# Kernel optimization log

Hardware: AMD Instinct MI355X
Metric: run time of the kernel (lower is better)

Reference implementation:

```python
import jax, jax.numpy as jnp
import numpy as np

N, DIN, D, H, L, S, E = 3072, 64, 128, 4, 2, 4, 49152
NEG = -2.0**32 + 1.0


def _layernorm(x, g, b, eps=1e-5):
    m = jnp.mean(x, axis=-1, keepdims=True)
    v = jnp.var(x, axis=-1, keepdims=True)
    return (x - m) * jax.lax.rsqrt(v + eps) * g + b


def setup_inputs() -> dict:
    key = jax.random.key(0)
    ks = jax.random.split(key, 24)
    w = lambda k, shp: (0.02 * jax.random.normal(k, shp)).astype(jnp.float32)
    inp = {
        "x": jax.random.normal(ks[0], (N, DIN), dtype=jnp.float32),
        "edge_index": jax.random.randint(ks[1], (2, E), 0, N, dtype=jnp.int64) if jax.config.jax_enable_x64 else jax.random.randint(ks[1], (2, E), 0, N).astype(jnp.int32),
        "shortest_path_len": jax.random.randint(ks[2], (N, N), 0, 11).astype(jnp.int32),
        "edge_feat": jax.random.normal(ks[3], (N, N, S), dtype=jnp.float32),
        # input projection
        "node_W": w(ks[4], (DIN, D)), "node_b": jnp.zeros((D,), jnp.float32),
        # centrality / spatial / edge encodings
        "deg_emb": w(ks[5], (N, D)),
        "sp_emb": w(ks[6], (11, 1)),
        "edge_W": w(ks[7], (S, S)), "edge_b": jnp.zeros((S,), jnp.float32),
        # per-layer stacked attention params
        "ln1_g": jnp.ones((L, D), jnp.float32), "ln1_b": jnp.zeros((L, D), jnp.float32),
        "Wq": w(ks[8], (L, H, D, D)), "bq": jnp.zeros((L, H, D), jnp.float32),
        "Wk": w(ks[9], (L, H, D, D)), "bk": jnp.zeros((L, H, D), jnp.float32),
        "Wv": w(ks[10], (L, H, D, D)), "bv": jnp.zeros((L, H, D), jnp.float32),
        "Wo": w(ks[11], (L, H * D, D)), "bo": jnp.zeros((L, D), jnp.float32),
        "ln2_g": jnp.ones((L, D), jnp.float32), "ln2_b": jnp.zeros((L, D), jnp.float32),
        "ff_W": w(ks[12], (L, D, D)), "ff_b": jnp.zeros((L, D), jnp.float32),
        # output projection
        "out_W": w(ks[13], (D, D)), "out_b": jnp.zeros((D,), jnp.float32),
    }
    return inp


def reference(x, edge_index, shortest_path_len, edge_feat,
              node_W, node_b, deg_emb, sp_emb, edge_W, edge_b,
              ln1_g, ln1_b, Wq, bq, Wk, bk, Wv, bv, Wo, bo,
              ln2_g, ln2_b, ff_W, ff_b, out_W, out_b):
    # padding mask from raw features
    mask_idx = (jnp.sum(x, axis=1) != 0).astype(x.dtype)            # [N]
    mask = mask_idx[:, None] * mask_idx[None, :]                    # [N,N]

    h = x @ node_W + node_b                                         # [N,D]
    # centrality: degree of edge destinations
    deg = jax.ops.segment_sum(jnp.ones((edge_index.shape[1],), jnp.int32),
                              edge_index[1], num_segments=N)        # [N]
    h = h + deg_emb[deg]

    spatial = sp_emb[shortest_path_len][..., 0]                     # [N,N]
    edge_m = (edge_feat @ edge_W + edge_b).mean(axis=-1)            # [N,N]
    bias = spatial + edge_m
    scale = 1.0 / jnp.sqrt(jnp.asarray(D, x.dtype))

    for l in range(L):
        x_ln = _layernorm(h, ln1_g[l], ln1_b[l])                    # [N,D]
        q = jnp.einsum('nd,hdk->hnk', x_ln, Wq[l]) + bq[l][:, None, :]
        k = jnp.einsum('nd,hdk->hnk', x_ln, Wk[l]) + bk[l][:, None, :]
        v = jnp.einsum('nd,hdk->hnk', x_ln, Wv[l]) + bv[l][:, None, :]
        a = jnp.einsum('hnk,hmk->hnm', q, k) * scale + bias[None]   # [H,N,N]
        a = jnp.where(mask[None] == 0, NEG, a)
        s = jax.nn.softmax(a, axis=-1)
        s = jnp.where(mask[None] == 0, 0.0, s)
        o = jnp.einsum('hnm,hmd->hnd', s, v)                        # [H,N,D]
        cat = jnp.transpose(o, (1, 0, 2)).reshape(N, H * D)         # [N,H*D]
        x_out = cat @ Wo[l] + bo[l] + h
        h = _layernorm(x_out, ln2_g[l], ln2_b[l]) @ ff_W[l] + ff_b[l] + x_out

    return h @ out_W + out_b
```

## Files before the change

kernel.cpp:

```cpp
#include <hip/hip_runtime.h>
#include <math.h>

static constexpr int N   = 3072;
static constexpr int DIN = 64;
static constexpr int D   = 128;
static constexpr int H   = 4;
static constexpr int E   = 49152;
#define NEGV  (-4294967295.0f)
#define SCALE (0.08838834764831845f)

typedef unsigned short u16;
typedef __attribute__((ext_vector_type(8))) short short8;
typedef __attribute__((ext_vector_type(4))) float f32x4;
typedef __attribute__((ext_vector_type(4))) unsigned short u16x4;

__device__ __forceinline__ u16 f2bf(float f){
  unsigned int u = __float_as_uint(f);
  u += 0x7fff + ((u >> 16) & 1);
  return (u16)(u >> 16);
}
__device__ __forceinline__ float bf2f(u16 u){
  return __uint_as_float(((unsigned int)u) << 16);
}

__global__ void k_zero_deg(int* __restrict__ deg){
  int i = blockIdx.x*blockDim.x + threadIdx.x;
  if(i < N) deg[i] = 0;
}

__global__ void k_deg(const int* __restrict__ ei, int* __restrict__ deg){
  int e = blockIdx.x*blockDim.x + threadIdx.x;
  if(e < E) atomicAdd(&deg[ei[E + e]], 1);
}

__global__ void k_h0(const float* __restrict__ x, const float* __restrict__ nodeW,
                     const float* __restrict__ nodeb, const float* __restrict__ degemb,
                     const int* __restrict__ deg, const float* __restrict__ g1,
                     const float* __restrict__ b1, float* __restrict__ mask,
                     float* __restrict__ h, float* __restrict__ xln){
  const int i = blockIdx.x, t = threadIdx.x;
  float xv = x[i*DIN + t];
  float s = xv;
  #pragma unroll
  for(int o=32;o;o>>=1) s += __shfl_xor(s, o);
  if(t == 0) mask[i] = (s != 0.0f) ? 1.0f : 0.0f;
  __shared__ float xr[DIN];
  xr[t] = xv;
  __syncthreads();
  int dg = deg[i]; dg = dg > N-1 ? N-1 : dg;
  float a0 = nodeb[t]      + degemb[dg*D + t];
  float a1 = nodeb[t + 64] + degemb[dg*D + t + 64];
  #pragma unroll
  for(int u=0; u<DIN; ++u){
    float xu = xr[u];
    a0 = fmaf(xu, nodeW[u*D + t],      a0);
    a1 = fmaf(xu, nodeW[u*D + t + 64], a1);
  }
  h[i*D + t]      = a0;
  h[i*D + t + 64] = a1;
  float s2 = a0 + a1, sq = a0*a0 + a1*a1;
  #pragma unroll
  for(int o=32;o;o>>=1){ s2 += __shfl_xor(s2, o); sq += __shfl_xor(sq, o); }
  float mean = s2*(1.0f/128.0f);
  float var  = sq*(1.0f/128.0f) - mean*mean;
  float inv  = rsqrtf(var + 1e-5f);
  xln[i*D + t]      = (a0 - mean)*inv*g1[t]      + b1[t];
  xln[i*D + t + 64] = (a1 - mean)*inv*g1[t + 64] + b1[t + 64];
}

__global__ void k_bias(const int* __restrict__ spl, const float* __restrict__ ef,
                       const float* __restrict__ spe, const float* __restrict__ eW,
                       const float* __restrict__ eb, const float* __restrict__ mask,
                       u16* __restrict__ biasm){
  int idx = blockIdx.x*blockDim.x + threadIdx.x;
  int i = idx / N, j = idx % N;
  float wm0 = (eW[0] + eW[1] + eW[2] + eW[3])  * 0.25f;
  float wm1 = (eW[4] + eW[5] + eW[6] + eW[7])  * 0.25f;
  float wm2 = (eW[8] + eW[9] + eW[10]+ eW[11]) * 0.25f;
  float wm3 = (eW[12]+ eW[13]+ eW[14]+ eW[15]) * 0.25f;
  float bm  = (eb[0] + eb[1] + eb[2] + eb[3])  * 0.25f;
  float4 e4 = reinterpret_cast<const float4*>(ef)[idx];
  float em = fmaf(e4.x, wm0, fmaf(e4.y, wm1, fmaf(e4.z, wm2, fmaf(e4.w, wm3, bm))));
  float b = spe[spl[idx]] + em;
  float mk = mask[i]*mask[j];
  biasm[idx] = f2bf((mk != 0.0f) ? b : NEGV);
}

__global__ __launch_bounds__(256) void k_wt_all(const float* __restrict__ Wq, const float* __restrict__ Wk,
    const float* __restrict__ Wv, const float* __restrict__ ffW, const float* __restrict__ outW,
    u16* __restrict__ wt_qkv, u16* __restrict__ wt_ff, u16* __restrict__ wt_out){
  __shared__ float t[32][33];
  const int z = blockIdx.y;
  const float* src; u16* dst;
  if(z < 24){
    int l = z/12, r = z%12;
    const float* W = (r>>2)==0 ? Wq : (r>>2)==1 ? Wk : Wv;
    src = W + (size_t)(l*4 + (r&3))*16384;
    dst = wt_qkv + (size_t)z*16384;
  } else if(z < 26){
    src = ffW + (size_t)(z-24)*16384; dst = wt_ff + (size_t)(z-24)*16384;
  } else { src = outW; dst = wt_out; }
  const int ki = blockIdx.x & 3, ni = blockIdx.x >> 2;
  const int tid = threadIdx.x;
  #pragma unroll
  for(int i=0;i<4;i++){
    int idx = tid + i*256, r = idx>>5, c = idx&31;
    t[r][c] = src[(size_t)(ki*32+r)*128 + ni*32 + c];
  }
  __syncthreads();
  #pragma unroll
  for(int i=0;i<4;i++){
    int idx = tid + i*256, r = idx>>5, c = idx&31;
    dst[(size_t)(ni*32+r)*128 + ki*32 + c] = f2bf(t[c][r]);
  }
}

__global__ __launch_bounds__(256) void k_wt_wo(const float* __restrict__ Wo, u16* __restrict__ wt_wo){
  __shared__ float t[32][33];
  const int l = blockIdx.y;
  const float* src = Wo + (size_t)l*65536;
  u16* dst = wt_wo + (size_t)l*65536;
  const int ki = blockIdx.x & 15, ni = blockIdx.x >> 4;
  const int tid = threadIdx.x;
  #pragma unroll
  for(int i=0;i<4;i++){
    int idx = tid + i*256, r = idx>>5, c = idx&31;
    t[r][c] = src[(size_t)(ki*32+r)*128 + ni*32 + c];
  }
  __syncthreads();
  #pragma unroll
  for(int i=0;i<4;i++){
    int idx = tid + i*256, r = idx>>5, c = idx&31;
    dst[(size_t)(ni*32+r)*512 + ki*32 + c] = f2bf(t[c][r]);
  }
}

template<int MODE>
__device__ __forceinline__ void mgemm_body(const float* __restrict__ A, const u16* __restrict__ Bt,
                                           const float* __restrict__ bias, void* __restrict__ Cv){
  __shared__ u16 As[64*128];
  __shared__ u16 Bs[128*128];
  const int tid = threadIdx.x, w = tid>>6, lane = tid&63;
  const int g4 = lane>>4, l16 = lane&15;
  const int m0 = blockIdx.x*64;
  const int srow = tid>>4, sch = tid&15;
  f32x4 acc[8];
  #pragma unroll
  for(int nt=0;nt<8;++nt) acc[nt] = (f32x4){0.f,0.f,0.f,0.f};
  #pragma unroll
  for(int it=0;it<4;++it){
    int row = it*16 + srow;
    const float4* ap = reinterpret_cast<const float4*>(A + (size_t)(m0+row)*128 + sch*8);
    float4 x0 = ap[0], x1 = ap[1];
    u16x4 p0, p1;
    p0.x=f2bf(x0.x); p0.y=f2bf(x0.y); p0.z=f2bf(x0.z); p0.w=f2bf(x0.w);
    p1.x=f2bf(x1.x); p1.y=f2bf(x1.y); p1.z=f2bf(x1.z); p1.w=f2bf(x1.w);
    u16* dst = &As[row*128 + ((sch ^ (row&15))*8)];
    *reinterpret_cast<u16x4*>(dst)     = p0;
    *reinterpret_cast<u16x4*>(dst + 4) = p1;
  }
  #pragma unroll
  for(int it=0;it<8;++it){
    int row = it*16 + srow;
    short8 b = *reinterpret_cast<const short8*>(Bt + (size_t)row*128 + sch*8);
    *reinterpret_cast<short8*>(&Bs[row*128 + ((sch ^ (row&15))*8)]) = b;
  }
  __syncthreads();
  __builtin_amdgcn_s_setprio(1);
  #pragma unroll
  for(int c=0;c<4;++c){
    short8 af = *reinterpret_cast<const short8*>(&As[(w*16+l16)*128 + (((c*4+g4) ^ l16)*8)]);
    #pragma unroll
    for(int nt=0;nt<8;++nt){
      short8 bf = *reinterpret_cast<const short8*>(&Bs[(nt*16+l16)*128 + (((c*4+g4) ^ l16)*8)]);
      acc[nt] = __builtin_amdgcn_mfma_f32_16x16x32_bf16(af, bf, acc[nt], 0, 0, 0);
    }
  }
  __builtin_amdgcn_s_setprio(0);
  const int mrow = m0 + w*16 + g4*4;
  if(MODE == 2){
    __syncthreads();
    u16* T = Bs;
    #pragma unroll
    for(int nt=0;nt<8;++nt){
      const int col = nt*16 + l16;
      float bi = bias[col];
      u16x4 t;
      t.x = f2bf(acc[nt][0] + bi); t.y = f2bf(acc[nt][1] + bi);
      t.z = f2bf(acc[nt][2] + bi); t.w = f2bf(acc[nt][3] + bi);
      *reinterpret_cast<u16x4*>(&T[col*68 + (w*16 + g4*4)]) = t;
    }
    __syncthreads();
    #pragma unroll
    for(int i=0;i<4;++i){
      int slot = tid + i*256;
      int col = slot >> 3, q = slot & 7;
      short8 v = *reinterpret_cast<const short8*>(&T[col*68 + q*8]);
      *reinterpret_cast<short8*>((u16*)Cv + (size_t)col*N + m0 + q*8) = v;
    }
  } else {
    #pragma unroll
    for(int nt=0;nt<8;++nt){
      const int col = nt*16 + l16;
      float bi = bias[col];
      #pragma unroll
      for(int rg=0;rg<4;++rg){
        float v = acc[nt][rg] + bi;
        ((u16*)Cv)[(size_t)(mrow+rg)*128 + col] = f2bf(v);
      }
    }
  }
}

__global__ __launch_bounds__(256) void k_mqkv(const float* __restrict__ xln, const u16* __restrict__ wt_qkv,
    const float* __restrict__ bq, const float* __restrict__ bk, const float* __restrict__ bv,
    u16* __restrict__ q, u16* __restrict__ k, u16* __restrict__ vT, int l){
  const int z = blockIdx.y, which = z>>2, head = z&3;
  const u16* Bt = wt_qkv + (size_t)(l*12 + z)*16384;
  if(which == 0)      mgemm_body<1>(xln, Bt, bq + (l*H+head)*D, q  + (size_t)head*N*D);
  else if(which == 1) mgemm_body<1>(xln, Bt, bk + (l*H+head)*D, k  + (size_t)head*N*D);
  else                mgemm_body<2>(xln, Bt, bv + (l*H+head)*D, vT + (size_t)head*N*D);
}

template<int S, bool LAST>
__global__ __launch_bounds__(256) void k_mwoff(const u16* __restrict__ opart, const float* __restrict__ mpart,
    const float* __restrict__ lpart, const float* __restrict__ mask, const u16* __restrict__ wt_wo_l,
    const float* __restrict__ bo_l, const float* __restrict__ hres,
    const u16* __restrict__ wt_ff_l, const float* __restrict__ ffb_l,
    const float* __restrict__ g2, const float* __restrict__ b2,
    float* __restrict__ hout, float* __restrict__ xlnout,
    const float* __restrict__ g1n, const float* __restrict__ b1n,
    const u16* __restrict__ wt_out_m, const float* __restrict__ outb_m,
    float* __restrict__ finalout){
  __shared__ u16 As[64*128];
  __shared__ u16 Bs[128*128];
  const int tid = threadIdx.x, w = tid>>6, lane = tid&63;
  const int g4 = lane>>4, l16 = lane&15;
  const int m0 = blockIdx.x*64;
  const int srow = tid>>4, sch = tid&15;
  f32x4 acc[8];
  #pragma unroll
  for(int nt=0;nt<8;++nt) acc[nt] = (f32x4){0.f,0.f,0.f,0.f};
  for(int k0 = 0; k0 < 512; k0 += 128){
    const int hh = k0 >> 7;
    __syncthreads();
    #pragma unroll
    for(int it=0;it<4;++it){
      int row = it*16 + srow;
      int grow = m0 + row;
      float w_[S]; float M = -INFINITY; float mv[S], lv[S];
      #pragma unroll
      for(int s=0;s<S;++s){
        mv[s] = mpart[(size_t)(s*H + hh)*N + grow];
        lv[s] = lpart[(size_t)(s*H + hh)*N + grow];
        M = fmaxf(M, mv[s]);
      }
      float denom = 0.f;
      #pragma unroll
      for(int s=0;s<S;++s){ w_[s] = __expf(mv[s] - M); denom = fmaf(lv[s], w_[s], denom); }
      float scale = mask[grow] / denom;
      const int d = sch*8;
      float v[8] = {0,0,0,0,0,0,0,0};
      #pragma unroll
      for(int s=0;s<S;++s){
        short8 ov = *reinterpret_cast<const short8*>(
            opart + ((size_t)(s*H + hh)*N + grow)*D + d);
        #pragma unroll
        for(int j=0;j<8;++j) v[j] = fmaf(bf2f((u16)ov[j]), w_[s], v[j]);
      }
      u16x4 p0, p1;
      p0.x=f2bf(v[0]*scale); p0.y=f2bf(v[1]*scale); p0.z=f2bf(v[2]*scale); p0.w=f2bf(v[3]*scale);
      p1.x=f2bf(v[4]*scale); p1.y=f2bf(v[5]*scale); p1.z=f2bf(v[6]*scale); p1.w=f2bf(v[7]*scale);
      u16* dst = &As[row*128 + ((sch ^ (row&15))*8)];
      *reinterpret_cast<u16x4*>(dst)     = p0;
      *reinterpret_cast<u16x4*>(dst + 4) = p1;
    }
    #pragma unroll
    for(int it=0;it<8;++it){
      int row = it*16 + srow;
      short8 b = *reinterpret_cast<const short8*>(wt_wo_l + (size_t)row*512 + k0 + sch*8);
      *reinterpret_cast<short8*>(&Bs[row*128 + ((sch ^ (row&15))*8)]) = b;
    }
    __syncthreads();
    __builtin_amdgcn_s_setprio(1);
    #pragma unroll
    for(int c=0;c<4;++c){
      short8 af = *reinterpret_cast<const short8*>(&As[(w*16+l16)*128 + (((c*4+g4) ^ l16)*8)]);
      #pragma unroll
      for(int nt=0;nt<8;++nt){
        short8 bf = *reinterpret_cast<const short8*>(&Bs[(nt*16+l16)*128 + (((c*4+g4) ^ l16)*8)]);
        acc[nt] = __builtin_amdgcn_mfma_f32_16x16x32_bf16(af, bf, acc[nt], 0, 0, 0);
      }
    }
    __builtin_amdgcn_s_setprio(0);
  }
  const int mrow = m0 + w*16 + g4*4;
  float s_[4] = {0,0,0,0}, q_[4] = {0,0,0,0};
  #pragma unroll
  for(int nt=0;nt<8;++nt){
    const int col = nt*16 + l16;
    float bi = bo_l[col];
    #pragma unroll
    for(int rg=0;rg<4;++rg){
      float v = acc[nt][rg] + bi + hres[(size_t)(mrow+rg)*128 + col];
      acc[nt][rg] = v;
      s_[rg] += v; q_[rg] = fmaf(v, v, q_[rg]);
    }
  }
  #pragma unroll
  for(int o=1;o<16;o<<=1){
    #pragma unroll
    for(int rg=0;rg<4;++rg){ s_[rg] += __shfl_xor(s_[rg], o); q_[rg] += __shfl_xor(q_[rg], o); }
  }
  float mean[4], inv[4];
  #pragma unroll
  for(int rg=0;rg<4;++rg){
    mean[rg] = s_[rg]*(1.0f/128.0f);
    float var = q_[rg]*(1.0f/128.0f) - mean[rg]*mean[rg];
    inv[rg] = rsqrtf(var + 1e-5f);
  }
  __syncthreads();
  #pragma unroll
  for(int nt=0;nt<8;++nt){
    const int col = nt*16 + l16;
    const int ch = col >> 3, wi = col & 7;
    float gg = g2[col], bb = b2[col];
    #pragma unroll
    for(int rg=0;rg<4;++rg){
      int row = w*16 + g4*4 + rg;
      As[row*128 + ((ch ^ (row&15))*8) + wi] = f2bf((acc[nt][rg] - mean[rg])*inv[rg]*gg + bb);
    }
  }
  #pragma unroll
  for(int it=0;it<8;++it){
    int row = it*16 + srow;
    short8 b = *reinterpret_cast<const short8*>(wt_ff_l + (size_t)row*128 + sch*8);
    *reinterpret_cast<short8*>(&Bs[row*128 + ((sch ^ (row&15))*8)]) = b;
  }
  __syncthreads();
  f32x4 acc2[8];
  #pragma unroll
  for(int nt=0;nt<8;++nt) acc2[nt] = (f32x4){0.f,0.f,0.f,0.f};
  __builtin_amdgcn_s_setprio(1);
  #pragma unroll
  for(int c=0;c<4;++c){
    short8 af = *reinterpret_cast<const short8*>(&As[(w*16+l16)*128 + (((c*4+g4) ^ l16)*8)]);
    #pragma unroll
    for(int nt=0;nt<8;++nt){
      short8 bf = *reinterpret_cast<const short8*>(&Bs[(nt*16+l16)*128 + (((c*4+g4) ^ l16)*8)]);
      acc2[nt] = __builtin_amdgcn_mfma_f32_16x16x32_bf16(af, bf, acc2[nt], 0, 0, 0);
    }
  }
  __builtin_amdgcn_s_setprio(0);
  #pragma unroll
  for(int nt=0;nt<8;++nt){
    const int col = nt*16 + l16;
    float bi = ffb_l[col];
    #pragma unroll
    for(int rg=0;rg<4;++rg)
      acc2[nt][rg] += bi + acc[nt][rg];
  }
  if(!LAST){
    float s2_[4] = {0,0,0,0}, q2_[4] = {0,0,0,0};
    #pragma unroll
    for(int nt=0;nt<8;++nt){
      const int col = nt*16 + l16;
      #pragma unroll
      for(int rg=0;rg<4;++rg){
        float v = acc2[nt][rg];
        hout[(size_t)(mrow+rg)*128 + col] = v;
        s2_[rg] += v; q2_[rg] = fmaf(v, v, q2_[rg]);
      }
    }
    #pragma unroll
    for(int o=1;o<16;o<<=1){
      #pragma unroll
      for(int rg=0;rg<4;++rg){ s2_[rg] += __shfl_xor(s2_[rg], o); q2_[rg] += __shfl_xor(q2_[rg], o); }
    }
    #pragma unroll
    for(int rg=0;rg<4;++rg){
      float mn = s2_[rg]*(1.0f/128.0f);
      float var = q2_[rg]*(1.0f/128.0f) - mn*mn;
      s2_[rg] = mn; q2_[rg] = rsqrtf(var + 1e-5f);
    }
    #pragma unroll
    for(int nt=0;nt<8;++nt){
      const int col = nt*16 + l16;
      float gg = g1n[col], bb = b1n[col];
      #pragma unroll
      for(int rg=0;rg<4;++rg)
        xlnout[(size_t)(mrow+rg)*128 + col] = (acc2[nt][rg] - s2_[rg])*q2_[rg]*gg + bb;
    }
  } else {
    __syncthreads();
    #pragma unroll
    for(int nt=0;nt<8;++nt){
      const int col = nt*16 + l16;
      const int ch = col >> 3, wi = col & 7;
      #pragma unroll
      for(int rg=0;rg<4;++rg){
        int row = w*16 + g4*4 + rg;
        As[row*128 + ((ch ^ (row&15))*8) + wi] = f2bf(acc2[nt][rg]);
      }
    }
    #pragma unroll
    for(int it=0;it<8;++it){
      int row = it*16 + srow;
      short8 b = *reinterpret_cast<const short8*>(wt_out_m + (size_t)row*128 + sch*8);
      *reinterpret_cast<short8*>(&Bs[row*128 + ((sch ^ (row&15))*8)]) = b;
    }
    __syncthreads();
    f32x4 acc3[8];
    #pragma unroll
    for(int nt=0;nt<8;++nt) acc3[nt] = (f32x4){0.f,0.f,0.f,0.f};
    __builtin_amdgcn_s_setprio(1);
    #pragma unroll
    for(int c=0;c<4;++c){
      short8 af = *reinterpret_cast<const short8*>(&As[(w*16+l16)*128 + (((c*4+g4) ^ l16)*8)]);
      #pragma unroll
      for(int nt=0;nt<8;++nt){
        short8 bf = *reinterpret_cast<const short8*>(&Bs[(nt*16+l16)*128 + (((c*4+g4) ^ l16)*8)]);
        acc3[nt] = __builtin_amdgcn_mfma_f32_16x16x32_bf16(af, bf, acc3[nt], 0, 0, 0);
      }
    }
    __builtin_amdgcn_s_setprio(0);
    #pragma unroll
    for(int nt=0;nt<8;++nt){
      const int col = nt*16 + l16;
      float bi = outb_m[col];
      #pragma unroll
      for(int rg=0;rg<4;++rg)
        finalout[(size_t)(mrow+rg)*128 + col] = acc3[nt][rg] + bi;
    }
  }
}

__global__ __launch_bounds__(256) void k_attn(const u16* __restrict__ q, const u16* __restrict__ k,
                     const u16* __restrict__ vT, const u16* __restrict__ biasm,
                     u16* __restrict__ opart, float* __restrict__ mpart, float* __restrict__ lpart,
                     int kvlen){
  const int tid  = threadIdx.x;
  const int w    = tid >> 6;
  const int lane = tid & 63;
  const int g4 = lane >> 4, l16 = lane & 15;
  const int head = blockIdx.y, sp = blockIdx.z;
  const int r0 = blockIdx.x*64 + w*16;
  __shared__ u16 Ks[64*128];
  __shared__ u16 Vs[64*128];
  __shared__ u16 P[4][16][40];

  const u16* qbase = q + ((size_t)head*N + r0)*D;
  short8 qf[4];
  #pragma unroll
  for(int c=0;c<4;c++)
    qf[c] = *reinterpret_cast<const short8*>(qbase + l16*D + c*32 + g4*8);

  f32x4 o[8];
  #pragma unroll
  for(int dt=0;dt<8;dt++) o[dt] = (f32x4){0.f,0.f,0.f,0.f};
  float m = -INFINITY, lsum = 0.0f;

  const u16* kh   = k  + (size_t)head*N*D;
  const u16* vTh  = vT + (size_t)head*D*N;
  const u16* brow = biasm + (size_t)(r0 + l16)*N;
  const int kv0 = sp*kvlen;

  const int krow = tid >> 4, kch = tid & 15;
  const int vrow = tid >> 3, vch = tid & 7;

  for(int j0 = kv0; j0 < kv0 + kvlen; j0 += 64){
    short8 kreg[4], vreg[4];
    #pragma unroll
    for(int it=0; it<4; ++it)
      kreg[it] = *reinterpret_cast<const short8*>(kh + (size_t)(j0 + it*16 + krow)*D + kch*8);
    #pragma unroll
    for(int it=0; it<4; ++it)
      vreg[it] = *reinterpret_cast<const short8*>(vTh + (size_t)(it*32 + vrow)*N + j0 + vch*8);
    u16x4 bb[4];
    #pragma unroll
    for(int z=0; z<4; ++z)
      bb[z] = *reinterpret_cast<const u16x4*>(brow + j0 + z*16 + g4*4);

    __syncthreads();
    #pragma unroll
    for(int it=0; it<4; ++it){
      int row = it*16 + krow;
      *reinterpret_cast<short8*>(&Ks[row*128 + ((kch ^ (row&15))*8)]) = kreg[it];
    }
    #pragma unroll
    for(int it=0; it<4; ++it){
      int d = it*32 + vrow;
      int row = d & 63, ch = ((d>>6)<<3) | vch;
      *reinterpret_cast<short8*>(&Vs[row*128 + ((ch ^ (row&15))*8)]) = vreg[it];
    }
    __syncthreads();

    #pragma unroll
    for(int ks=0; ks<2; ++ks){
      short8 kf[8];
      const int rowA = ks*32 + l16, rowB = rowA + 16;
      #pragma unroll
      for(int c=0;c<4;c++){
        kf[c]   = *reinterpret_cast<const short8*>(&Ks[rowA*128 + (((c*4+g4) ^ l16)*8)]);
        kf[4+c] = *reinterpret_cast<const short8*>(&Ks[rowB*128 + (((c*4+g4) ^ l16)*8)]);
      }
      f32x4 sA = (f32x4){0.f,0.f,0.f,0.f}, sB = sA;
      __builtin_amdgcn_s_setprio(1);
      #pragma unroll
      for(int c=0;c<4;c++){
        sA = __builtin_amdgcn_mfma_f32_16x16x32_bf16(kf[c],   qf[c], sA, 0, 0, 0);
        sB = __builtin_amdgcn_mfma_f32_16x16x32_bf16(kf[4+c], qf[c], sB, 0, 0, 0);
      }
      __builtin_amdgcn_s_setprio(0);
      u16x4 bA = bb[2*ks], bB = bb[2*ks+1];
      sA[0] = fmaf(sA[0], SCALE, bf2f(bA.x)); sA[1] = fmaf(sA[1], SCALE, bf2f(bA.y));
      sA[2] = fmaf(sA[2], SCALE, bf2f(bA.z)); sA[3] = fmaf(sA[3], SCALE, bf2f(bA.w));
      sB[0] = fmaf(sB[0], SCALE, bf2f(bB.x)); sB[1] = fmaf(sB[1], SCALE, bf2f(bB.y));
      sB[2] = fmaf(sB[2], SCALE, bf2f(bB.z)); sB[3] = fmaf(sB[3], SCALE, bf2f(bB.w));
      float pmax = fmaxf(fmaxf(fmaxf(sA[0],sA[1]), fmaxf(sA[2],sA[3])),
                         fmaxf(fmaxf(sB[0],sB[1]), fmaxf(sB[2],sB[3])));
      pmax = fmaxf(pmax, __shfl_xor(pmax, 16));
      pmax = fmaxf(pmax, __shfl_xor(pmax, 32));
      if(!__all(pmax - m <= 8.0f)){
        float mnew = fmaxf(m, pmax);
        float corr = __expf(m - mnew);
        lsum *= corr;
        float c0 = __shfl(corr, (lane & 48) | (g4*4 + 0));
        float c1 = __shfl(corr, (lane & 48) | (g4*4 + 1));
        float c2 = __shfl(corr, (lane & 48) | (g4*4 + 2));
        float c3 = __shfl(corr, (lane & 48) | (g4*4 + 3));
        #pragma unroll
        for(int dt=0;dt<8;dt++){
          o[dt][0] *= c0; o[dt][1] *= c1; o[dt][2] *= c2; o[dt][3] *= c3;
        }
        m = mnew;
      }
      f32x4 pA, pB;
      #pragma unroll
      for(int rg=0;rg<4;rg++){ pA[rg] = __expf(sA[rg] - m); pB[rg] = __expf(sB[rg] - m); }
      float ps = (pA[0]+pA[1]) + (pA[2]+pA[3]) + ((pB[0]+pB[1]) + (pB[2]+pB[3]));
      ps += __shfl_xor(ps, 16);
      ps += __shfl_xor(ps, 32);
      lsum += ps;
      u16x4 wa, wb;
      wa.x = f2bf(pA[0]); wa.y = f2bf(pA[1]); wa.z = f2bf(pA[2]); wa.w = f2bf(pA[3]);
      wb.x = f2bf(pB[0]); wb.y = f2bf(pB[1]); wb.z = f2bf(pB[2]); wb.w = f2bf(pB[3]);
      *reinterpret_cast<u16x4*>(&P[w][l16][g4*4])      = wa;
      *reinterpret_cast<u16x4*>(&P[w][l16][16 + g4*4]) = wb;
      short8 pf = *reinterpret_cast<const short8*>(&P[w][l16][g4*8]);
      __builtin_amdgcn_s_setprio(1);
      #pragma unroll
      for(int dt=0;dt<8;dt++){
        int d = dt*16 + l16;
        int row = d & 63;
        int ch  = ((dt>>2)<<3) | (ks<<2) | g4;
        short8 vf = *reinterpret_cast<const short8*>(&Vs[row*128 + ((ch ^ l16)*8)]);
        o[dt] = __builtin_amdgcn_mfma_f32_16x16x32_bf16(pf, vf, o[dt], 0, 0, 0);
      }
      __builtin_amdgcn_s_setprio(0);
    }
  }

  u16* ob = opart + ((size_t)((sp*H + head)*N) + r0)*D;
  #pragma unroll
  for(int dt=0;dt<8;dt++){
    #pragma unroll
    for(int rg=0;rg<4;rg++)
      ob[(size_t)(g4*4+rg)*D + dt*16 + l16] = f2bf(o[dt][rg]);
  }
  if(g4 == 0){
    mpart[(size_t)(sp*H + head)*N + r0 + l16] = m;
    lpart[(size_t)(sp*H + head)*N + r0 + l16] = lsum;
  }
}

extern "C" void kernel_launch(void* const* d_in, const int* in_sizes, int n_in,
                              void* d_out, int out_size, void* d_ws, size_t ws_size,
                              hipStream_t stream){
  const float* x      = (const float*)d_in[0];
  const int*   ei     = (const int*)  d_in[1];
  const int*   spl    = (const int*)  d_in[2];
  const float* ef     = (const float*)d_in[3];
  const float* nodeW  = (const float*)d_in[4];
  const float* nodeb  = (const float*)d_in[5];
  const float* degemb = (const float*)d_in[6];
  const float* spe    = (const float*)d_in[7];
  const float* eW     = (const float*)d_in[8];
  const float* eb     = (const float*)d_in[9];
  const float* ln1g   = (const float*)d_in[10];
  const float* ln1b   = (const float*)d_in[11];
  const float* Wq     = (const float*)d_in[12];
  const float* bq     = (const float*)d_in[13];
  const float* Wk     = (const float*)d_in[14];
  const float* bk     = (const float*)d_in[15];
  const float* Wv     = (const float*)d_in[16];
  const float* bv     = (const float*)d_in[17];
  const float* Wo     = (const float*)d_in[18];
  const float* bo     = (const float*)d_in[19];
  const float* ln2g   = (const float*)d_in[20];
  const float* ln2b   = (const float*)d_in[21];
  const float* ffW    = (const float*)d_in[22];
  const float* ffb    = (const float*)d_in[23];
  const float* outW   = (const float*)d_in[24];
  const float* outb   = (const float*)d_in[25];

  constexpr size_t WT_ELEMS = 24*16384 + 2*16384 + 16384 + 2*65536;
  auto needed = [](int s)->size_t{
    size_t fl = 8192 + 3*(size_t)N*D;
    size_t bf = 3*(size_t)H*N*D + (size_t)N*N + (size_t)s*H*N*D;
    size_t pf = 2*(size_t)s*H*N;
    return fl*4 + bf*2 + pf*4 + WT_ELEMS*2;
  };
  int S = 2;
  if(needed(8) <= ws_size) S = 8;
  else if(needed(4) <= ws_size) S = 4;

  float* ws   = (float*)d_ws;
  int*   deg  = (int*)ws;
  float* mask = ws + 4096;
  float* h    = ws + 8192;
  float* xln  = h    + N*D;
  float* xout = xln  + N*D;
  u16*   qb   = (u16*)(xout + N*D);
  u16*   kb   = qb + (size_t)H*N*D;
  u16*   vTb  = kb + (size_t)H*N*D;
  u16*   biasm= vTb + (size_t)H*N*D;
  u16*   opart= biasm + (size_t)N*N;
  float* mpart= (float*)(opart + (size_t)S*H*N*D);
  float* lpart= mpart + (size_t)S*H*N;
  u16*   wt_qkv = (u16*)(lpart + (size_t)S*H*N);
  u16*   wt_ff  = wt_qkv + 24*16384;
  u16*   wt_out = wt_ff  + 2*16384;
  u16*   wt_wo  = wt_out + 16384;

  k_wt_all<<<dim3(16, 27), 256, 0, stream>>>(Wq, Wk, Wv, ffW, outW, wt_qkv, wt_ff, wt_out);
  k_wt_wo<<<dim3(64, 2), 256, 0, stream>>>(Wo, wt_wo);
  k_zero_deg<<<(N+255)/256, 256, 0, stream>>>(deg);
  k_deg<<<(E+255)/256, 256, 0, stream>>>(ei, deg);
  k_h0<<<N, 64, 0, stream>>>(x, nodeW, nodeb, degemb, deg, ln1g, ln1b, mask, h, xln);
  k_bias<<<(N*N)/256, 256, 0, stream>>>(spl, ef, spe, eW, eb, mask, biasm);

  for(int l = 0; l < 2; ++l){
    k_mqkv<<<dim3(N/64, 12), 256, 0, stream>>>(xln, wt_qkv, bq, bk, bv, qb, kb, vTb, l);
    k_attn<<<dim3(N/64, H, S), 256, 0, stream>>>(qb, kb, vTb, biasm, opart, mpart, lpart, N/S);
    const u16* wwo = wt_wo + (size_t)l*65536;
    const u16* wff = wt_ff + (size_t)l*16384;
    if(l == 0){
      if(S == 8)
        k_mwoff<8,false><<<N/64, 256, 0, stream>>>(opart, mpart, lpart, mask, wwo, bo + l*D, h,
            wff, ffb + l*D, ln2g + l*D, ln2b + l*D, h, xln, ln1g + D, ln1b + D,
            nullptr, nullptr, nullptr);
      else if(S == 4)
        k_mwoff<4,false><<<N/64, 256, 0, stream>>>(opart, mpart, lpart, mask, wwo, bo + l*D, h,
            wff, ffb + l*D, ln2g + l*D, ln2b + l*D, h, xln, ln1g + D, ln1b + D,
            nullptr, nullptr, nullptr);
      else
        k_mwoff<2,false><<<N/64, 256, 0, stream>>>(opart, mpart, lpart, mask, wwo, bo + l*D, h,
            wff, ffb + l*D, ln2g + l*D, ln2b + l*D, h, xln, ln1g + D, ln1b + D,
            nullptr, nullptr, nullptr);
    } else {
      if(S == 8)
        k_mwoff<8,true><<<N/64, 256, 0, stream>>>(opart, mpart, lpart, mask, wwo, bo + l*D, h,
            wff, ffb + l*D, ln2g + l*D, ln2b + l*D, nullptr, nullptr, nullptr, nullptr,
            wt_out, outb, (float*)d_out);
      else if(S == 4)
        k_mwoff<4,true><<<N/64, 256, 0, stream>>>(opart, mpart, lpart, mask, wwo, bo + l*D, h,
            wff, ffb + l*D, ln2g + l*D, ln2b + l*D, nullptr, nullptr, nullptr, nullptr,
            wt_out, outb, (float*)d_out);
      else
        k_mwoff<2,true><<<N/64, 256, 0, stream>>>(opart, mpart, lpart, mask, wwo, bo + l*D, h,
            wff, ffb + l*D, ln2g + l*D, ln2b + l*D, nullptr, nullptr, nullptr, nullptr,
            wt_out, outb, (float*)d_out);
    }
  }
}
```

Measured before the change: 219.8 us.

## Double-buffer K/V tiles in attention using direct global-to-LDS async loads

The attention kernel now stages K and V tiles straight into shared memory with global_load_lds. It double-buffers them, prefetching the next 64-key tile and its bias values while MFMAs run on the current tile. This removes the register round-trip and the second barrier per iteration, and is meant to hide global load latency behind compute. In exchange, shared memory per block roughly doubles, which can lower occupancy. Correctness depends on the barrier waiting for the outstanding async LDS loads.

```diff
diff --git a/kernel.cpp b/kernel.cpp
--- a/kernel.cpp
+++ b/kernel.cpp
@@ -21,6 +21,12 @@
 }
 __device__ __forceinline__ float bf2f(u16 u){
   return __uint_as_float(((unsigned int)u) << 16);
+}
+
+__device__ __forceinline__ void gl_lds16(const void* g, void* l){
+  __builtin_amdgcn_global_load_lds(
+      (const __attribute__((address_space(1))) void*)g,
+      (__attribute__((address_space(3))) void*)l, 16, 0, 0);
 }
 
 __global__ void k_zero_deg(int* __restrict__ deg){
@@ -445,8 +451,8 @@
   const int g4 = lane >> 4, l16 = lane & 15;
   const int head = blockIdx.y, sp = blockIdx.z;
   const int r0 = blockIdx.x*64 + w*16;
-  __shared__ u16 Ks[64*128];
-  __shared__ u16 Vs[64*128];
+  __shared__ u16 Ks[2][64*128];
+  __shared__ u16 Vs[2][64*128];
   __shared__ u16 P[4][16][40];
 
   const u16* qbase = q + ((size_t)head*N + r0)*D;
@@ -465,44 +471,54 @@
   const u16* brow = biasm + (size_t)(r0 + l16)*N;
   const int kv0 = sp*kvlen;
 
-  const int krow = tid >> 4, kch = tid & 15;
-  const int vrow = tid >> 3, vch = tid & 7;
-
+  const int srow4 = lane >> 4;
+  const int sch16 = lane & 15;
+  const int rl    = w*4 + srow4;
+  const int kc    = sch16 ^ rl;
+  const int vch0  = sch16 ^ rl;
+  const int vd_lo = ((vch0 & 8) << 3) + rl;
+
+  auto stage = [&](int jt, int buf){
+    #pragma unroll
+    for(int it=0; it<4; ++it){
+      const u16* ksrc = kh + (size_t)(jt + it*16 + rl)*D + kc*8;
+      gl_lds16(ksrc, &Ks[buf][(size_t)(it*16 + w*4)*128]);
+    }
+    #pragma unroll
+    for(int it=0; it<4; ++it){
+      const u16* vsrc = vTh + (size_t)(vd_lo + it*16)*N + jt + (vch0 & 7)*8;
+      gl_lds16(vsrc, &Vs[buf][(size_t)(it*16 + w*4)*128]);
+    }
+  };
+
+  u16x4 bb[4];
+  #pragma unroll
+  for(int z=0; z<4; ++z)
+    bb[z] = *reinterpret_cast<const u16x4*>(brow + kv0 + z*16 + g4*4);
+  stage(kv0, 0);
+
+  int cur = 0;
   for(int j0 = kv0; j0 < kv0 + kvlen; j0 += 64){
-    short8 kreg[4], vreg[4];
-    #pragma unroll
-    for(int it=0; it<4; ++it)
-      kreg[it] = *reinterpret_cast<const short8*>(kh + (size_t)(j0 + it*16 + krow)*D + kch*8);
-    #pragma unroll
-    for(int it=0; it<4; ++it)
-      vreg[it] = *reinterpret_cast<const short8*>(vTh + (size_t)(it*32 + vrow)*N + j0 + vch*8);
-    u16x4 bb[4];
-    #pragma unroll
-    for(int z=0; z<4; ++z)
-      bb[z] = *reinterpret_cast<const u16x4*>(brow + j0 + z*16 + g4*4);
-
     __syncthreads();
-    #pragma unroll
-    for(int it=0; it<4; ++it){
-      int row = it*16 + krow;
-      *reinterpret_cast<short8*>(&Ks[row*128 + ((kch ^ (row&15))*8)]) = kreg[it];
-    }
-    #pragma unroll
-    for(int it=0; it<4; ++it){
-      int d = it*32 + vrow;
-      int row = d & 63, ch = ((d>>6)<<3) | vch;
-      *reinterpret_cast<short8*>(&Vs[row*128 + ((ch ^ (row&15))*8)]) = vreg[it];
-    }
-    __syncthreads();
-
+    const bool has_next = (j0 + 64 < kv0 + kvlen);
+    u16x4 bbn[4];
+    if(has_next){
+      #pragma unroll
+      for(int z=0; z<4; ++z)
+        bbn[z] = *reinterpret_cast<const u16x4*>(brow + j0 + 64 + z*16 + g4*4);
+      stage(j0 + 64, cur ^ 1);
+    }
+
+    const u16* KsC = Ks[cur];
+    const u16* VsC = Vs[cur];
     #pragma unroll
     for(int ks=0; ks<2; ++ks){
       short8 kf[8];
       const int rowA = ks*32 + l16, rowB = rowA + 16;
       #pragma unroll
       for(int c=0;c<4;c++){
-        kf[c]   = *reinterpret_cast<const short8*>(&Ks[rowA*128 + (((c*4+g4) ^ l16)*8)]);
-        kf[4+c] = *reinterpret_cast<const short8*>(&Ks[rowB*128 + (((c*4+g4) ^ l16)*8)]);
+        kf[c]   = *reinterpret_cast<const short8*>(&KsC[rowA*128 + (((c*4+g4) ^ l16)*8)]);
+        kf[4+c] = *reinterpret_cast<const short8*>(&KsC[rowB*128 + (((c*4+g4) ^ l16)*8)]);
       }
       f32x4 sA = (f32x4){0.f,0.f,0.f,0.f}, sB = sA;
       __builtin_amdgcn_s_setprio(1);
@@ -554,11 +570,16 @@
         int d = dt*16 + l16;
         int row = d & 63;
         int ch  = ((dt>>2)<<3) | (ks<<2) | g4;
-        short8 vf = *reinterpret_cast<const short8*>(&Vs[row*128 + ((ch ^ l16)*8)]);
+        short8 vf = *reinterpret_cast<const short8*>(&VsC[row*128 + ((ch ^ l16)*8)]);
         o[dt] = __builtin_amdgcn_mfma_f32_16x16x32_bf16(pf, vf, o[dt], 0, 0, 0);
       }
       __builtin_amdgcn_s_setprio(0);
     }
+    if(has_next){
+      #pragma unroll
+      for(int z=0; z<4; ++z) bb[z] = bbn[z];
+    }
+    cur ^= 1;
   }
 
   u16* ob = opart + ((size_t)((sp*H + head)*N) + r0)*D;
```

After: 244.9 us. +11.4%, slower.
